# Optimization experiments

Measured on AMD Instinct MI355X. Metric: run time of the kernel, lower is better.

## Reference

```python
import jax, jax.numpy as jnp
import numpy as np

DIL = 1  # dilation


def setup_inputs() -> dict:
    key = jax.random.key(0)
    k0, k1, k2, k3 = jax.random.split(key, 4)
    B, Cin, Cout, K, L, NR = 16, 256, 256, 3, 4096, 5
    x = jax.random.normal(k0, (B, Cin, L), jnp.float32)
    # kaiming-uniform-ish scale for conv kernels
    base_kernels = jax.random.normal(k1, (NR, Cout, Cin, K), jnp.float32) * (1.0 / np.sqrt(Cin * K))
    base_biases = jax.random.normal(k2, (NR, Cout), jnp.float32) * (1.0 / np.sqrt(Cin * K))
    # controller: Linear(Cin*K -> NR) followed by softmax over rules
    ctrl_w = jax.random.normal(k3, (Cin * K, NR), jnp.float32) * (1.0 / np.sqrt(Cin * K))
    ctrl_b = jnp.zeros((NR,), jnp.float32)
    return {"x": x, "base_kernels": base_kernels, "base_biases": base_biases,
            "ctrl_w": ctrl_w, "ctrl_b": ctrl_b}


def reference(x, base_kernels, base_biases, ctrl_w, ctrl_b):
    NR, Cout, Cin, K = base_kernels.shape
    B, _, L = x.shape
    pad = (K - 1) * DIL
    px = jnp.pad(x, ((0, 0), (0, 0), (pad, 0)))  # causal left pad -> (B, Cin, L+pad)

    # patches: padded_x.unfold(dim=2, size=K, step=1)[:, :, :L] -> (B, Cin, L, K)
    patches = jnp.stack([px[:, :, k:k + L] for k in range(K)], axis=-1)
    patches = patches.transpose(0, 2, 1, 3).reshape(B, L, Cin * K)  # (B, L, Cin*K)

    # controller -> normalized firing strengths (B, L, NR)
    fr = jax.nn.softmax(patches @ ctrl_w + ctrl_b, axis=-1)

    # all n_rules causal convs in one grouped-as-batched-output conv
    rhs = base_kernels.reshape(NR * Cout, Cin, K)
    conv = jax.lax.conv_general_dilated(
        px, rhs, window_strides=(1,), padding=[(0, 0)],
        rhs_dilation=(DIL,), dimension_numbers=("NCH", "OIH", "NCH"))  # (B, NR*Cout, L)
    conv = conv.reshape(B, NR, Cout, L) + base_biases[None, :, :, None]

    # weighted sum over experts: sum_n fr[b,l,n] * conv[b,n,o,l]
    return jnp.einsum("bnol,bln->bol", conv, fr)
```

## Files before the change

### kernel.cpp

```cpp
#include <hip/hip_runtime.h>
#include <hip/hip_bf16.h>

typedef __attribute__((ext_vector_type(4))) float floatx4;
typedef __attribute__((ext_vector_type(8))) short shortx8;

#define NB   16
#define CIN  256
#define COUT 256
#define KW   3
#define LL   4096
#define LLP  4098
#define NR   5
#define QK   768
#define NP   65536

static __device__ __forceinline__ unsigned short bf16bits(float f) {
    __hip_bfloat16 h = __float2bfloat16(f);
    return __builtin_bit_cast(unsigned short, h);
}

static __device__ __forceinline__ void gload16(const void* g, void* l) {
    __builtin_amdgcn_global_load_lds(
        (const __attribute__((address_space(1))) void*)g,
        (__attribute__((address_space(3))) void*)l, 16, 0, 0);
}

__global__ void k_tfr(const float* __restrict__ x, const float* __restrict__ cw,
                      const float* __restrict__ cb, const float* __restrict__ bk,
                      __hip_bfloat16* __restrict__ wb,
                      __hip_bfloat16* __restrict__ xt, float* __restrict__ fr) {
    __shared__ float t[66][65];
    __shared__ float cwsh[QK * NR];
    int l0 = blockIdx.x * 64, b = blockIdx.y;
    int bid = blockIdx.y * 64 + blockIdx.x;
    int tid = threadIdx.x;
    int r16 = tid >> 4, q16 = tid & 15;
    int p = tid >> 2, q = tid & 3;

    #pragma unroll
    for (int jj = 0; jj < 4; ++jj) {
        int i = bid * 1024 + jj * 256 + tid;
        if (i < NR * COUT * QK) {
            int m = i / QK, qq = i % QK;
            int o = (m / 80) * 16 + (m & 15);
            int r = (m % 80) / 16;
            int k = qq >> 8, cin = qq & 255;
            wb[i] = __float2bfloat16(bk[((r * COUT + o) * CIN + cin) * KW + k]);
        }
    }
    {
        int i0 = bid * 256 + tid;
        if (i0 < NB * 2 * CIN) {
            int bb = i0 >> 9, rr = i0 & 511;
            xt[(size_t)bb * LLP * CIN + rr] = __float2bfloat16(0.f);
        }
    }

    for (int i = tid; i < QK * NR; i += 256) cwsh[i] = cw[i];

    float lg[NR] = {0.f, 0.f, 0.f, 0.f, 0.f};
    for (int ch = 0; ch < 4; ++ch) {
        __syncthreads();
        #pragma unroll
        for (int pass = 0; pass < 4; ++pass) {
            int cin = pass * 16 + r16;
            float4 v = *(const float4*)&x[((size_t)(b * CIN + ch * 64 + cin)) * LL + l0 + q16 * 4];
            t[q16 * 4 + 2][cin] = v.x;
            t[q16 * 4 + 3][cin] = v.y;
            t[q16 * 4 + 4][cin] = v.z;
            t[q16 * 4 + 5][cin] = v.w;
        }
        if (tid < 128) {
            int cin = tid >> 1, j = tid & 1;
            float v = 0.f;
            if (l0 > 0) v = x[((size_t)(b * CIN + ch * 64 + cin)) * LL + l0 - 2 + j];
            t[j][cin] = v;
        }
        __syncthreads();

        #pragma unroll
        for (int pass = 0; pass < 4; ++pass) {
            int lr = pass * 16 + r16;
            int c4 = q16 * 4;
            ushort4 u;
            u.x = bf16bits(t[lr + 2][c4 + 0]);
            u.y = bf16bits(t[lr + 2][c4 + 1]);
            u.z = bf16bits(t[lr + 2][c4 + 2]);
            u.w = bf16bits(t[lr + 2][c4 + 3]);
            *(ushort4*)&xt[((size_t)(b * LLP + 2 + l0 + lr)) * CIN + ch * 64 + c4] = u;
        }

        #pragma unroll 4
        for (int ci = 0; ci < 16; ++ci) {
            int cin = q * 16 + ci;
            float x0 = t[p][cin], x1 = t[p + 1][cin], x2 = t[p + 2][cin];
            const float* w = &cwsh[(ch * 64 + cin) * 3 * NR];
            #pragma unroll
            for (int n = 0; n < NR; ++n)
                lg[n] += x0 * w[n] + x1 * w[NR + n] + x2 * w[2 * NR + n];
        }
    }
    #pragma unroll
    for (int n = 0; n < NR; ++n) {
        lg[n] += __shfl_xor(lg[n], 1);
        lg[n] += __shfl_xor(lg[n], 2);
    }
    if (q == 0) {
        float l2[NR];
        #pragma unroll
        for (int n = 0; n < NR; ++n) l2[n] = lg[n] + cb[n];
        float m = l2[0];
        #pragma unroll
        for (int n = 1; n < NR; ++n) m = fmaxf(m, l2[n]);
        float e[NR], s = 0.f;
        #pragma unroll
        for (int n = 0; n < NR; ++n) { e[n] = __expf(l2[n] - m); s += e[n]; }
        float inv = 1.f / s;
        #pragma unroll
        for (int n = 0; n < NR; ++n) fr[(size_t)(b * LL + l0 + p) * NR + n] = e[n] * inv;
    }
}

#define XBUF  8256
#define WBUF  7680
#define WOFF  24768
__global__ __launch_bounds__(256, 2)
void k_conv(const __hip_bfloat16* __restrict__ xt, const __hip_bfloat16* __restrict__ wb,
            const float* __restrict__ fr, const float* __restrict__ bias,
            float* __restrict__ out) {
    __shared__ __align__(16) short lds[3 * XBUF + 2 * WBUF];
    __shared__ float bs[80];

    int g = blockIdx.x;
    int pt = ((g >> 7) << 3) | (g & 7);
    int y  = (g >> 3) & 15;
    int p0 = pt * 256;
    int m0 = y * 80, o0 = y * 16;
    int b = p0 >> 12, l0 = p0 & (LL - 1);
    int tid = threadIdx.x;
    int lane = tid & 63, wn = tid >> 6;
    int quad = lane >> 4, l16 = lane & 15;

    const __hip_bfloat16* xb = xt + (size_t)b * (LLP * CIN);

    if (tid < 80) bs[tid] = bias[(tid >> 4) * COUT + o0 + (tid & 15)];

    int xchk[5];
    #pragma unroll
    for (int j = 0; j < 4; ++j) xchk[j] = j * 256 + tid;
    xchk[4] = 968 + lane;
    int xsrc[5];
    #pragma unroll
    for (int j = 0; j < 5; ++j) {
        int c = xchk[j];
        int row = c >> 2, cs = c & 3;
        int cg = cs ^ ((row >> 1) & 3);
        xsrc[j] = (l0 + row) * CIN + cg * 8;
    }
    int wchk[4];
    #pragma unroll
    for (int j = 0; j < 3; ++j) wchk[j] = j * 256 + tid;
    wchk[3] = 704 + tid;
    int wsrc[4];
    #pragma unroll
    for (int j = 0; j < 4; ++j) {
        int c = wchk[j];
        int s = c >> 2, cs = c & 3;
        int cg = cs ^ ((s >> 1) & 3);
        int kh = s / 80, m = s - kh * 80;
        wsrc[j] = (m0 + m) * QK + kh * 256 + cg * 8;
    }

    int boff[3][4], aoff[3][5];
    #pragma unroll
    for (int kh = 0; kh < 3; ++kh) {
        #pragma unroll
        for (int nf = 0; nf < 4; ++nf) {
            int row = wn * 64 + nf * 16 + l16 + kh;
            boff[kh][nf] = row * 32 + (quad ^ ((row >> 1) & 3)) * 8;
        }
        #pragma unroll
        for (int mf = 0; mf < NR; ++mf) {
            int s = kh * 80 + mf * 16 + l16;
            aoff[kh][mf] = s * 32 + (quad ^ ((s >> 1) & 3)) * 8;
        }
    }

    floatx4 acc[NR][4];
    #pragma unroll
    for (int mf = 0; mf < NR; ++mf)
        #pragma unroll
        for (int nf = 0; nf < 4; ++nf)
            acc[mf][nf] = (floatx4){0.f, 0.f, 0.f, 0.f};

    auto stageX = [&](int buf, int ph) {
        short* B = &lds[buf * XBUF];
        const __hip_bfloat16* xp = xb + ph * 32;
        #pragma unroll
        for (int j = 0; j < 5; ++j)
            gload16(xp + xsrc[j], B + xchk[j] * 8);
    };
    auto stageW = [&](int buf, int ph) {
        short* B = &lds[WOFF + buf * WBUF];
        const __hip_bfloat16* wp = wb + ph * 32;
        #pragma unroll
        for (int j = 0; j < 4; ++j)
            gload16(wp + wsrc[j], B + wchk[j] * 8);
    };

    auto compute = [&](int ph) {
        const short* X = &lds[(ph % 3) * XBUF];
        const short* W = &lds[WOFF + (ph & 1) * WBUF];
        #pragma unroll
        for (int kh = 0; kh < 3; ++kh) {
            shortx8 bfrag[4], afrag[NR];
            #pragma unroll
            for (int nf = 0; nf < 4; ++nf)
                bfrag[nf] = *(const shortx8*)&X[boff[kh][nf]];
            #pragma unroll
            for (int mf = 0; mf < NR; ++mf)
                afrag[mf] = *(const shortx8*)&W[aoff[kh][mf]];
            #pragma unroll
            for (int mf = 0; mf < NR; ++mf)
                #pragma unroll
                for (int nf = 0; nf < 4; ++nf)
                    acc[mf][nf] = __builtin_amdgcn_mfma_f32_16x16x32_bf16(
                        afrag[mf], bfrag[nf], acc[mf][nf], 0, 0, 0);
        }
    };

    stageW(0, 0); stageX(0, 0); stageX(1, 1);
    #pragma unroll
    for (int ph = 0; ph < 8; ++ph) {
        if (ph == 0)      asm volatile("s_waitcnt vmcnt(5) lgkmcnt(0)" ::: "memory");
        else if (ph < 7)  asm volatile("s_waitcnt vmcnt(5)" ::: "memory");
        else              asm volatile("s_waitcnt vmcnt(0)" ::: "memory");
        __builtin_amdgcn_s_barrier();
        __builtin_amdgcn_sched_barrier(0);
        if (ph < 7) stageW((ph + 1) & 1, ph + 1);
        if (ph < 6) stageX((ph + 2) % 3, ph + 2);
        __builtin_amdgcn_s_setprio(1);
        compute(ph);
        __builtin_amdgcn_s_setprio(0);
    }

    #pragma unroll
    for (int nf = 0; nf < 4; ++nf) {
        int colp = wn * 64 + nf * 16 + l16;
        const float* fp = fr + (size_t)(p0 + colp) * NR;
        float f0 = fp[0], f1 = fp[1], f2 = fp[2], f3 = fp[3], f4 = fp[4];
        #pragma unroll
        for (int j = 0; j < 4; ++j) {
            int olo = quad * 4 + j;
            float v = f0 * (acc[0][nf][j] + bs[0 * 16 + olo])
                    + f1 * (acc[1][nf][j] + bs[1 * 16 + olo])
                    + f2 * (acc[2][nf][j] + bs[2 * 16 + olo])
                    + f3 * (acc[3][nf][j] + bs[3 * 16 + olo])
                    + f4 * (acc[4][nf][j] + bs[4 * 16 + olo]);
            out[((size_t)(b * COUT + o0 + olo)) * LL + l0 + colp] = v;
        }
    }
}

extern "C" void kernel_launch(void* const* d_in, const int* in_sizes, int n_in,
                              void* d_out, int out_size, void* d_ws, size_t ws_size,
                              hipStream_t stream) {
    const float* x  = (const float*)d_in[0];
    const float* bk = (const float*)d_in[1];
    const float* bb = (const float*)d_in[2];
    const float* cw = (const float*)d_in[3];
    const float* cb = (const float*)d_in[4];
    float* out = (float*)d_out;

    char* ws = (char*)d_ws;
    __hip_bfloat16* xt = (__hip_bfloat16*)ws;
    __hip_bfloat16* wb = (__hip_bfloat16*)(ws + 33570816);
    float*          fr = (float*)(ws + 33570816 + 1966080);

    k_tfr<<<dim3(LL / 64, NB), dim3(256), 0, stream>>>(x, cw, cb, bk, wb, xt, fr);
    k_conv<<<dim3(NP / 256 * (COUT / 16)), dim3(256), 0, stream>>>(xt, wb, fr, bb, out);
}
```

Before: 259.9 us.

## Fold controller logits into conv MFMA as extra M-tile, compute softmax in epilogue

The controller projection is packed as an extra 16-row bf16 weight tile, so each conv block computes the rule logits with MFMA alongside the expert convolutions. The softmax then runs in the epilogue through a small LDS exchange. This removes the scalar fp32 logit loop and the fr round-trip from the prep kernel. In exchange, every one of the 16 output-channel blocks recomputes the logits, adding about a fifth more MFMA work. The logits are now computed in bf16 rather than fp32. The pipeline also drops from 3-stage X buffering with hand-tuned waitcnt/setprio to plain double buffering with __syncthreads, which may expose more load latency.

```diff
diff --git a/kernel.cpp b/kernel.cpp
--- a/kernel.cpp
+++ b/kernel.cpp
@@ -25,17 +25,15 @@
         (__attribute__((address_space(3))) void*)l, 16, 0, 0);
 }
 
-__global__ void k_tfr(const float* __restrict__ x, const float* __restrict__ cw,
-                      const float* __restrict__ cb, const float* __restrict__ bk,
-                      __hip_bfloat16* __restrict__ wb,
-                      __hip_bfloat16* __restrict__ xt, float* __restrict__ fr) {
-    __shared__ float t[66][65];
-    __shared__ float cwsh[QK * NR];
+__global__ void k_tfr(const float* __restrict__ x, const float* __restrict__ bk,
+                      const float* __restrict__ cw,
+                      __hip_bfloat16* __restrict__ wb, __hip_bfloat16* __restrict__ wc,
+                      __hip_bfloat16* __restrict__ xt) {
+    __shared__ float t[64][65];
     int l0 = blockIdx.x * 64, b = blockIdx.y;
     int bid = blockIdx.y * 64 + blockIdx.x;
     int tid = threadIdx.x;
     int r16 = tid >> 4, q16 = tid & 15;
-    int p = tid >> 2, q = tid & 3;
 
     #pragma unroll
     for (int jj = 0; jj < 4; ++jj) {
@@ -48,6 +46,12 @@
             wb[i] = __float2bfloat16(bk[((r * COUT + o) * CIN + cin) * KW + k]);
         }
     }
+    if (bid < 48) {
+        int row = bid, cin = tid;
+        int kh = row >> 4, r = row & 15;
+        float v = (r < NR) ? cw[(cin * 3 + kh) * NR + r] : 0.f;
+        wc[row * 256 + cin] = __float2bfloat16(v);
+    }
     {
         int i0 = bid * 256 + tid;
         if (i0 < NB * 2 * CIN) {
@@ -56,79 +60,40 @@
         }
     }
 
-    for (int i = tid; i < QK * NR; i += 256) cwsh[i] = cw[i];
-
-    float lg[NR] = {0.f, 0.f, 0.f, 0.f, 0.f};
     for (int ch = 0; ch < 4; ++ch) {
         __syncthreads();
         #pragma unroll
         for (int pass = 0; pass < 4; ++pass) {
             int cin = pass * 16 + r16;
             float4 v = *(const float4*)&x[((size_t)(b * CIN + ch * 64 + cin)) * LL + l0 + q16 * 4];
-            t[q16 * 4 + 2][cin] = v.x;
-            t[q16 * 4 + 3][cin] = v.y;
-            t[q16 * 4 + 4][cin] = v.z;
-            t[q16 * 4 + 5][cin] = v.w;
-        }
-        if (tid < 128) {
-            int cin = tid >> 1, j = tid & 1;
-            float v = 0.f;
-            if (l0 > 0) v = x[((size_t)(b * CIN + ch * 64 + cin)) * LL + l0 - 2 + j];
-            t[j][cin] = v;
+            t[q16 * 4 + 0][cin] = v.x;
+            t[q16 * 4 + 1][cin] = v.y;
+            t[q16 * 4 + 2][cin] = v.z;
+            t[q16 * 4 + 3][cin] = v.w;
         }
         __syncthreads();
-
         #pragma unroll
         for (int pass = 0; pass < 4; ++pass) {
             int lr = pass * 16 + r16;
             int c4 = q16 * 4;
             ushort4 u;
-            u.x = bf16bits(t[lr + 2][c4 + 0]);
-            u.y = bf16bits(t[lr + 2][c4 + 1]);
-            u.z = bf16bits(t[lr + 2][c4 + 2]);
-            u.w = bf16bits(t[lr + 2][c4 + 3]);
+            u.x = bf16bits(t[lr][c4 + 0]);
+            u.y = bf16bits(t[lr][c4 + 1]);
+            u.z = bf16bits(t[lr][c4 + 2]);
+            u.w = bf16bits(t[lr][c4 + 3]);
             *(ushort4*)&xt[((size_t)(b * LLP + 2 + l0 + lr)) * CIN + ch * 64 + c4] = u;
         }
-
-        #pragma unroll 4
-        for (int ci = 0; ci < 16; ++ci) {
-            int cin = q * 16 + ci;
-            float x0 = t[p][cin], x1 = t[p + 1][cin], x2 = t[p + 2][cin];
-            const float* w = &cwsh[(ch * 64 + cin) * 3 * NR];
-            #pragma unroll
-            for (int n = 0; n < NR; ++n)
-                lg[n] += x0 * w[n] + x1 * w[NR + n] + x2 * w[2 * NR + n];
-        }
-    }
-    #pragma unroll
-    for (int n = 0; n < NR; ++n) {
-        lg[n] += __shfl_xor(lg[n], 1);
-        lg[n] += __shfl_xor(lg[n], 2);
-    }
-    if (q == 0) {
-        float l2[NR];
-        #pragma unroll
-        for (int n = 0; n < NR; ++n) l2[n] = lg[n] + cb[n];
-        float m = l2[0];
-        #pragma unroll
-        for (int n = 1; n < NR; ++n) m = fmaxf(m, l2[n]);
-        float e[NR], s = 0.f;
-        #pragma unroll
-        for (int n = 0; n < NR; ++n) { e[n] = __expf(l2[n] - m); s += e[n]; }
-        float inv = 1.f / s;
-        #pragma unroll
-        for (int n = 0; n < NR; ++n) fr[(size_t)(b * LL + l0 + p) * NR + n] = e[n] * inv;
     }
 }
 
 #define XBUF  8256
-#define WBUF  7680
-#define WOFF  24768
+#define WBUF2 9216
+#define WOFF2 16512
 __global__ __launch_bounds__(256, 2)
 void k_conv(const __hip_bfloat16* __restrict__ xt, const __hip_bfloat16* __restrict__ wb,
-            const float* __restrict__ fr, const float* __restrict__ bias,
-            float* __restrict__ out) {
-    __shared__ __align__(16) short lds[3 * XBUF + 2 * WBUF];
+            const __hip_bfloat16* __restrict__ wc, const float* __restrict__ bias,
+            const float* __restrict__ cbv, float* __restrict__ out) {
+    __shared__ __align__(16) short lds[2 * XBUF + 2 * WBUF2];
     __shared__ float bs[80];
 
     int g = blockIdx.x;
@@ -144,6 +109,9 @@
     const __hip_bfloat16* xb = xt + (size_t)b * (LLP * CIN);
 
     if (tid < 80) bs[tid] = bias[(tid >> 4) * COUT + o0 + (tid & 15)];
+    float cbl[NR];
+    #pragma unroll
+    for (int n = 0; n < NR; ++n) cbl[n] = cbv[n];
 
     int xchk[5];
     #pragma unroll
@@ -157,21 +125,22 @@
         int cg = cs ^ ((row >> 1) & 3);
         xsrc[j] = (l0 + row) * CIN + cg * 8;
     }
-    int wchk[4];
-    #pragma unroll
-    for (int j = 0; j < 3; ++j) wchk[j] = j * 256 + tid;
-    wchk[3] = 704 + tid;
-    int wsrc[4];
-    #pragma unroll
-    for (int j = 0; j < 4; ++j) {
+    int wchk[5];
+    #pragma unroll
+    for (int j = 0; j < 4; ++j) wchk[j] = j * 256 + tid;
+    wchk[4] = 1024 + (tid & 127);
+    const __hip_bfloat16* wp[5];
+    #pragma unroll
+    for (int j = 0; j < 5; ++j) {
         int c = wchk[j];
         int s = c >> 2, cs = c & 3;
         int cg = cs ^ ((s >> 1) & 3);
-        int kh = s / 80, m = s - kh * 80;
-        wsrc[j] = (m0 + m) * QK + kh * 256 + cg * 8;
-    }
-
-    int boff[3][4], aoff[3][5];
+        int kh = s / 96, mp = s - kh * 96;
+        wp[j] = (mp < 80) ? wb + ((m0 + mp) * QK + kh * 256 + cg * 8)
+                          : wc + ((kh * 16 + mp - 80) * 256 + cg * 8);
+    }
+
+    int boff[3][4], aoff[3][6];
     #pragma unroll
     for (int kh = 0; kh < 3; ++kh) {
         #pragma unroll
@@ -180,48 +149,45 @@
             boff[kh][nf] = row * 32 + (quad ^ ((row >> 1) & 3)) * 8;
         }
         #pragma unroll
-        for (int mf = 0; mf < NR; ++mf) {
-            int s = kh * 80 + mf * 16 + l16;
+        for (int mf = 0; mf < 6; ++mf) {
+            int s = kh * 96 + mf * 16 + l16;
             aoff[kh][mf] = s * 32 + (quad ^ ((s >> 1) & 3)) * 8;
         }
     }
 
-    floatx4 acc[NR][4];
-    #pragma unroll
-    for (int mf = 0; mf < NR; ++mf)
+    floatx4 acc[6][4];
+    #pragma unroll
+    for (int mf = 0; mf < 6; ++mf)
         #pragma unroll
         for (int nf = 0; nf < 4; ++nf)
             acc[mf][nf] = (floatx4){0.f, 0.f, 0.f, 0.f};
 
-    auto stageX = [&](int buf, int ph) {
-        short* B = &lds[buf * XBUF];
+    auto stage = [&](int buf, int ph) {
+        short* BX = &lds[buf * XBUF];
         const __hip_bfloat16* xp = xb + ph * 32;
         #pragma unroll
         for (int j = 0; j < 5; ++j)
-            gload16(xp + xsrc[j], B + xchk[j] * 8);
+            gload16(xp + xsrc[j], BX + xchk[j] * 8);
+        short* BW = &lds[WOFF2 + buf * WBUF2];
+        #pragma unroll
+        for (int j = 0; j < 5; ++j)
+            gload16(wp[j] + ph * 32, BW + wchk[j] * 8);
     };
-    auto stageW = [&](int buf, int ph) {
-        short* B = &lds[WOFF + buf * WBUF];
-        const __hip_bfloat16* wp = wb + ph * 32;
-        #pragma unroll
-        for (int j = 0; j < 4; ++j)
-            gload16(wp + wsrc[j], B + wchk[j] * 8);
-    };
-
-    auto compute = [&](int ph) {
-        const short* X = &lds[(ph % 3) * XBUF];
-        const short* W = &lds[WOFF + (ph & 1) * WBUF];
+
+    auto compute = [&](int buf) {
+        const short* X = &lds[buf * XBUF];
+        const short* W = &lds[WOFF2 + buf * WBUF2];
         #pragma unroll
         for (int kh = 0; kh < 3; ++kh) {
-            shortx8 bfrag[4], afrag[NR];
+            shortx8 bfrag[4], afrag[6];
             #pragma unroll
             for (int nf = 0; nf < 4; ++nf)
                 bfrag[nf] = *(const shortx8*)&X[boff[kh][nf]];
             #pragma unroll
-            for (int mf = 0; mf < NR; ++mf)
+            for (int mf = 0; mf < 6; ++mf)
                 afrag[mf] = *(const shortx8*)&W[aoff[kh][mf]];
             #pragma unroll
-            for (int mf = 0; mf < NR; ++mf)
+            for (int mf = 0; mf < 6; ++mf)
                 #pragma unroll
                 for (int nf = 0; nf < 4; ++nf)
                     acc[mf][nf] = __builtin_amdgcn_mfma_f32_16x16x32_bf16(
@@ -229,26 +195,46 @@
         }
     };
 
-    stageW(0, 0); stageX(0, 0); stageX(1, 1);
+    stage(0, 0);
+    __syncthreads();
     #pragma unroll
     for (int ph = 0; ph < 8; ++ph) {
-        if (ph == 0)      asm volatile("s_waitcnt vmcnt(5) lgkmcnt(0)" ::: "memory");
-        else if (ph < 7)  asm volatile("s_waitcnt vmcnt(5)" ::: "memory");
-        else              asm volatile("s_waitcnt vmcnt(0)" ::: "memory");
-        __builtin_amdgcn_s_barrier();
-        __builtin_amdgcn_sched_barrier(0);
-        if (ph < 7) stageW((ph + 1) & 1, ph + 1);
-        if (ph < 6) stageX((ph + 2) % 3, ph + 2);
-        __builtin_amdgcn_s_setprio(1);
-        compute(ph);
-        __builtin_amdgcn_s_setprio(0);
-    }
+        if (ph < 7) stage((ph + 1) & 1, ph + 1);
+        compute(ph & 1);
+        __syncthreads();
+    }
+
+    float* scf = (float*)lds;
+    int pb = wn * 576;
+    #pragma unroll
+    for (int nf = 0; nf < 4; ++nf) {
+        int pp = pb + (nf * 16 + l16) * 9;
+        if (quad == 0) {
+            scf[pp + 0] = acc[5][nf][0];
+            scf[pp + 1] = acc[5][nf][1];
+            scf[pp + 2] = acc[5][nf][2];
+            scf[pp + 3] = acc[5][nf][3];
+        } else if (quad == 1) {
+            scf[pp + 4] = acc[5][nf][0];
+        }
+    }
+    __syncthreads();
 
     #pragma unroll
     for (int nf = 0; nf < 4; ++nf) {
         int colp = wn * 64 + nf * 16 + l16;
-        const float* fp = fr + (size_t)(p0 + colp) * NR;
-        float f0 = fp[0], f1 = fp[1], f2 = fp[2], f3 = fp[3], f4 = fp[4];
+        int pp = pb + (nf * 16 + l16) * 9;
+        float l2[NR];
+        #pragma unroll
+        for (int n = 0; n < NR; ++n) l2[n] = scf[pp + n] + cbl[n];
+        float mx = l2[0];
+        #pragma unroll
+        for (int n = 1; n < NR; ++n) mx = fmaxf(mx, l2[n]);
+        float e[NR], s = 0.f;
+        #pragma unroll
+        for (int n = 0; n < NR; ++n) { e[n] = __expf(l2[n] - mx); s += e[n]; }
+        float inv = 1.f / s;
+        float f0 = e[0] * inv, f1 = e[1] * inv, f2 = e[2] * inv, f3 = e[3] * inv, f4 = e[4] * inv;
         #pragma unroll
         for (int j = 0; j < 4; ++j) {
             int olo = quad * 4 + j;
@@ -275,8 +261,8 @@
     char* ws = (char*)d_ws;
     __hip_bfloat16* xt = (__hip_bfloat16*)ws;
     __hip_bfloat16* wb = (__hip_bfloat16*)(ws + 33570816);
-    float*          fr = (float*)(ws + 33570816 + 1966080);
-
-    k_tfr<<<dim3(LL / 64, NB), dim3(256), 0, stream>>>(x, cw, cb, bk, wb, xt, fr);
-    k_conv<<<dim3(NP / 256 * (COUT / 16)), dim3(256), 0, stream>>>(xt, wb, fr, bb, out);
-}
+    __hip_bfloat16* wc = (__hip_bfloat16*)(ws + 33570816 + 1966080);
+
+    k_tfr<<<dim3(LL / 64, NB), dim3(256), 0, stream>>>(x, bk, cw, wb, wc, xt);
+    k_conv<<<dim3(NP / 256 * (COUT / 16)), dim3(256), 0, stream>>>(xt, wb, wc, bb, cb, out);
+}
```

Measured after the change: 253.9 us. -2.3%, faster.
